# Performance work log

Hardware: AMD Instinct MI355X
Metric: run time of the kernel (lower is better)

Reference implementation:

```python
import jax, jax.numpy as jnp
import numpy as np
from jax import lax

DIM = 256; NH = 8; WS = 4; HD = DIM // NH  # head_dim=32
LH = 4; HH = 4; L_DIM = LH * HD; H_DIM = HH * HD  # 128 each
SCALE = HD ** -0.5


def conv2d(x, w, b, padding=0, groups=1):
    y = lax.conv_general_dilated(x, w, (1, 1), [(padding, padding)] * 2,
                                 feature_group_count=groups,
                                 dimension_numbers=('NCHW', 'OIHW', 'NCHW'))
    return y + b[None, :, None, None]


def dsc(x, dww, dwb, pww, pwb):
    # depthwise 3x3 (pad 1) + pointwise 1x1, both with bias
    y = conv2d(x, dww, dwb, padding=1, groups=x.shape[1])
    return conv2d(y, pww, pwb)


def setup_inputs() -> dict:
    key = jax.random.key(0)
    ks = jax.random.split(key, 16)
    p = lambda k, s: jax.random.normal(k, s, jnp.float32) * 0.02
    B, H, W = 8, 96, 96
    return {
        'x': jax.random.normal(ks[0], (B, DIM, H, W), jnp.float32),
        'restore_w': p(ks[1], (DIM, DIM // (WS * WS), 1, 1)), 'restore_b': jnp.zeros((DIM,), jnp.float32),
        'lq_dw_w': p(ks[2], (DIM, 1, 3, 3)), 'lq_dw_b': jnp.zeros((DIM,), jnp.float32),
        'lq_pw_w': p(ks[3], (L_DIM, DIM, 1, 1)), 'lq_pw_b': jnp.zeros((L_DIM,), jnp.float32),
        'lkv_dw_w': p(ks[4], (DIM, 1, 3, 3)), 'lkv_dw_b': jnp.zeros((DIM,), jnp.float32),
        'lkv_pw_w': p(ks[5], (2 * L_DIM, DIM, 1, 1)), 'lkv_pw_b': jnp.zeros((2 * L_DIM,), jnp.float32),
        'lproj_dw_w': p(ks[6], (L_DIM, 1, 3, 3)), 'lproj_dw_b': jnp.zeros((L_DIM,), jnp.float32),
        'lproj_pw_w': p(ks[7], (L_DIM, L_DIM, 1, 1)), 'lproj_pw_b': jnp.zeros((L_DIM,), jnp.float32),
        'hqkv_dw_w': p(ks[8], (DIM, 1, 3, 3)), 'hqkv_dw_b': jnp.zeros((DIM,), jnp.float32),
        'hqkv_pw_w': p(ks[9], (3 * H_DIM, DIM, 1, 1)), 'hqkv_pw_b': jnp.zeros((3 * H_DIM,), jnp.float32),
        'hproj_dw_w': p(ks[10], (H_DIM, 1, 3, 3)), 'hproj_dw_b': jnp.zeros((H_DIM,), jnp.float32),
        'hproj_pw_w': p(ks[11], (H_DIM, H_DIM, 1, 1)), 'hproj_pw_b': jnp.zeros((H_DIM,), jnp.float32),
    }


def reference(x, restore_w, restore_b,
              lq_dw_w, lq_dw_b, lq_pw_w, lq_pw_b,
              lkv_dw_w, lkv_dw_b, lkv_pw_w, lkv_pw_b,
              lproj_dw_w, lproj_dw_b, lproj_pw_w, lproj_pw_b,
              hqkv_dw_w, hqkv_dw_b, hqkv_pw_w, hqkv_pw_b,
              hproj_dw_w, hproj_dw_b, hproj_pw_w, hproj_pw_b):
    B, C, H, W = x.shape
    hg, wg = H // WS, W // WS
    # ---- low/high feature split (avg-pool + PixelShuffle fallback branch) ----
    low = jnp.mean(x.reshape(B, C, hg, WS, wg, WS), axis=(3, 5))  # [B,C,hg,wg]
    c_out = C // (WS * WS)
    lu = low.reshape(B, c_out, WS, WS, hg, wg)
    lu = lu.transpose(0, 1, 4, 2, 5, 3).reshape(B, c_out, H, W)  # PixelShuffle(WS)
    high = conv2d(lu, restore_w, restore_b) - x
    # ---- low-frequency (global) attention: q at full res, kv at pooled res ----
    lq = dsc(x, lq_dw_w, lq_dw_b, lq_pw_w, lq_pw_b)
    lq = lq.reshape(B, LH, HD, H * W).transpose(0, 1, 3, 2)  # [B,LH,HW,HD]
    lkv = dsc(low, lkv_dw_w, lkv_dw_b, lkv_pw_w, lkv_pw_b)
    lkv = lkv.reshape(B, 2, LH, HD, hg * wg).transpose(1, 0, 2, 4, 3)
    lk, lv = lkv[0], lkv[1]  # [B,LH,hg*wg,HD]
    l_attn = jax.nn.softmax(jnp.einsum('bhqd,bhkd->bhqk', lq, lk) * SCALE, axis=-1)
    lx = jnp.einsum('bhqk,bhkd->bhqd', l_attn, lv)  # [B,LH,HW,HD]
    lx = lx.transpose(0, 1, 3, 2).reshape(B, L_DIM, H, W)
    lx = dsc(lx, lproj_dw_w, lproj_dw_b, lproj_pw_w, lproj_pw_b)
    # ---- high-frequency (windowed local) attention ----
    qkv = dsc(high, hqkv_dw_w, hqkv_dw_b, hqkv_pw_w, hqkv_pw_b)
    qkv = qkv.reshape(B, 3 * HH, HD, hg, WS, wg, WS)
    qkv = qkv.transpose(0, 3, 5, 1, 4, 6, 2).reshape(B, hg * wg, 3, HH, WS * WS, HD)
    qkv = qkv.transpose(2, 0, 1, 3, 4, 5)
    hq, hk, hv = qkv[0], qkv[1], qkv[2]  # [B,G,HH,ws2,HD]
    h_attn = jax.nn.softmax(jnp.einsum('bgnqd,bgnkd->bgnqk', hq, hk) * SCALE, axis=-1)
    ho = jnp.einsum('bgnqk,bgnkd->bgnqd', h_attn, hv)  # [B,G,HH,ws2,HD]
    ho = ho.transpose(0, 1, 3, 2, 4).reshape(B, hg, wg, WS, WS, H_DIM)
    ho = ho.transpose(0, 1, 3, 2, 4, 5).reshape(B, H, W, H_DIM).transpose(0, 3, 1, 2)
    hx = dsc(ho, hproj_dw_w, hproj_dw_b, hproj_pw_w, hproj_pw_b)
    return jnp.concatenate([lx, hx], axis=1)  # [B,DIM,H,W]
```

## Files before the change

### kernel.cpp

```cpp
#include <hip/hip_runtime.h>


#define SCALE_F 0.17677669529663687f

typedef unsigned short u16;
typedef __attribute__((ext_vector_type(8))) short bf16x8;
typedef __attribute__((ext_vector_type(4))) float f32x4;
typedef __attribute__((ext_vector_type(8))) u16 u16x8;
typedef __attribute__((ext_vector_type(4))) u16 u16x4;

static __device__ __forceinline__ u16 f2bf(float f) {
    unsigned u = __float_as_uint(f);
    return (u16)((u + 0x7FFF + ((u >> 16) & 1)) >> 16);
}
static __device__ __forceinline__ float bf2f(u16 v) {
    return __uint_as_float((unsigned)v << 16);
}
static __device__ __forceinline__ float ldf(float v) { return v; }
static __device__ __forceinline__ float ldf(u16 v)   { return bf2f(v); }

__global__ __launch_bounds__(256) void pool_kernel(const float* __restrict__ x,
                                                   float* __restrict__ low) {
    int o = blockIdx.x * 256 + threadIdx.x;
    int wg = o % 24;
    int t  = o / 24;
    int hg = t % 24;
    int bc = t / 24;
    const float* xp = x + (size_t)bc * 9216 + (hg * 4) * 96 + wg * 4;
    float s = 0.f;
#pragma unroll
    for (int r = 0; r < 4; r++) {
        float4 v = *(const float4*)(xp + r * 96);
        s += (v.x + v.y) + (v.z + v.w);
    }
    low[o] = s * (1.f / 16.f);
}

__global__ __launch_bounds__(256) void high_kernel(const float* __restrict__ x,
                                                   const float* __restrict__ low,
                                                   const float* __restrict__ rw,
                                                   const float* __restrict__ rb,
                                                   u16* __restrict__ high) {
    int px = blockIdx.x * 256 + threadIdx.x;
    int cg = blockIdx.y;
    int b  = blockIdx.z;
    int h = px / 96, w = px % 96;
    int sub = (h & 3) * 4 + (w & 3);
    const float* lp = low + ((size_t)b * 256 + sub) * 576 + (h >> 2) * 24 + (w >> 2);
    float lv[16];
#pragma unroll
    for (int co = 0; co < 16; co++) lv[co] = lp[(size_t)co * 16 * 576];
    const float* xp = x    + ((size_t)b * 256 + cg * 64) * 9216 + px;
    u16*         hp = high + ((size_t)b * 256 + cg * 64) * 9216 + px;
#pragma unroll 4
    for (int cl = 0; cl < 64; cl++) {
        int c = cg * 64 + cl;
        float a = rb[c] - xp[(size_t)cl * 9216];
#pragma unroll
        for (int co = 0; co < 16; co++)
            a = fmaf(rw[c * 16 + co], lv[co], a);
        hp[(size_t)cl * 9216] = f2bf(a);
    }
}

__global__ __launch_bounds__(256) void wcvt_kernel(const float* __restrict__ s0,
                                                   const float* __restrict__ s1,
                                                   const float* __restrict__ s2,
                                                   const float* __restrict__ s3,
                                                   const float* __restrict__ s4,
                                                   u16* __restrict__ W) {
    int i = blockIdx.x * 256 + threadIdx.x;
    float v;
    if      (i < 32768)  v = s0[i];
    else if (i < 98304)  v = s1[i - 32768];
    else if (i < 114688) v = s2[i - 98304];
    else if (i < 212992) v = s3[i - 114688];
    else                 v = s4[i - 212992];
    W[i] = f2bf(v);
}

template <int C, int IMH, int IMW, typename TIN>
__global__ __launch_bounds__(256) void dw_kernel(const TIN* __restrict__ in,
                                                 const float* __restrict__ dww,
                                                 const float* __restrict__ dwb,
                                                 u16* __restrict__ Y) {
    constexpr int HW = IMH * IMW;
    constexpr int NSTRIP = HW / 8;
    const int strip = blockIdx.x * 32 + (threadIdx.x >> 3);
    if (strip >= NSTRIP) return;
    const int icq = threadIdx.x & 7;
    const int icg = blockIdx.y, b = blockIdx.z;
    const int ic  = icg * 8 + icq;
    const int px0 = strip * 8;
    const int h   = px0 / IMW, w0 = px0 % IMW;

    const TIN* ip = in + ((size_t)b * C + ic) * HW;
    float r[3][8], lh[3], rh[3];
#pragma unroll
    for (int dr = 0; dr < 3; dr++) {
        int hh = h + dr - 1;
        if (hh < 0 || hh >= IMH) {
#pragma unroll
            for (int j = 0; j < 8; j++) r[dr][j] = 0.f;
            lh[dr] = 0.f; rh[dr] = 0.f;
        } else {
            const TIN* rp = ip + hh * IMW + w0;
            if constexpr (sizeof(TIN) == 4) {
                float4 a = *(const float4*)rp;
                float4 c = *(const float4*)(rp + 4);
                r[dr][0] = a.x; r[dr][1] = a.y; r[dr][2] = a.z; r[dr][3] = a.w;
                r[dr][4] = c.x; r[dr][5] = c.y; r[dr][6] = c.z; r[dr][7] = c.w;
            } else {
                u16x8 a = *(const u16x8*)rp;
#pragma unroll
                for (int j = 0; j < 8; j++) r[dr][j] = bf2f(a[j]);
            }
            lh[dr] = (w0 > 0)           ? ldf(rp[-1]) : 0.f;
            rh[dr] = (w0 + 8 < IMW)     ? ldf(rp[8])  : 0.f;
        }
    }
    const float* wp = dww + ic * 9;
    float wv[9];
#pragma unroll
    for (int t = 0; t < 9; t++) wv[t] = wp[t];
    const float b0 = dwb[ic];

    u16* op = Y + (((size_t)b * (C / 8) + icg) * HW + px0) * 8 + icq;
#pragma unroll
    for (int j = 0; j < 8; j++) {
        float y = b0;
#pragma unroll
        for (int dr = 0; dr < 3; dr++) {
            float l = (j == 0) ? lh[dr] : r[dr][j - 1];
            float m = r[dr][j];
            float rr = (j == 7) ? rh[dr] : r[dr][j + 1];
            y = fmaf(wv[dr * 3 + 0], l, y);
            y = fmaf(wv[dr * 3 + 1], m, y);
            y = fmaf(wv[dr * 3 + 2], rr, y);
        }
        op[j * 8] = f2bf(y);
    }
}

template <int IC, int M, typename TOUT, int MODE>
__global__ __launch_bounds__(256) void pw_gemm(const u16* __restrict__ Y,
                                               const u16* __restrict__ Wmat,
                                               const float* __restrict__ bias,
                                               TOUT* __restrict__ out,
                                               int totc, int ocoff,
                                               u16* __restrict__ qkout,
                                               u16* __restrict__ vout) {
    const int tid  = threadIdx.x;
    const int wave = tid >> 6, lane = tid & 63;
    const int col  = lane & 15, oct = lane >> 4;
    const int mw   = (wave & 1) * 64, nw = (wave >> 1) * 64;
    const int px0    = blockIdx.x * 128;
    const int octile = blockIdx.y;
    const int b      = blockIdx.z;

    __shared__ union {
        struct { u16 W[128 * 72]; u16 Y[8 * 128 * 8]; } g;
        u16 stage[4][64 * 72];
    } lds;
    u16* const Wlds = lds.g.W;
    u16* const Ylds = lds.g.Y;

    f32x4 acc[4][4];
    const f32x4 zero = {0.f, 0.f, 0.f, 0.f};
#pragma unroll
    for (int i = 0; i < 4; i++)
#pragma unroll
        for (int j = 0; j < 4; j++) acc[i][j] = zero;

    const u16* Yb = Y + (size_t)b * (IC / 8) * M * 8;

    for (int kc = 0; kc < IC; kc += 64) {
        __syncthreads();
#pragma unroll
        for (int i = 0; i < 4; i++) {
            int c = tid + i * 256;
            int r = c >> 3, seg = c & 7;
            u16x8 v = *(const u16x8*)(Wmat + (size_t)(octile * 128 + r) * IC + kc + seg * 8);
            *(u16x8*)&Wlds[r * 72 + seg * 8] = v;
        }
#pragma unroll
        for (int i = 0; i < 4; i++) {
            int c = tid + i * 256;
            int ig = c >> 7, pl = c & 127;
            int px = px0 + pl; if (px > M - 1) px = M - 1;
            u16x8 v = *(const u16x8*)(Yb + ((size_t)(kc / 8 + ig) * M + px) * 8);
            *(u16x8*)&Ylds[(ig * 128 + pl) * 8] = v;
        }
        __syncthreads();
#pragma unroll
        for (int kcs = 0; kcs < 2; kcs++) {
            bf16x8 Af[4], Bf[4];
#pragma unroll
            for (int mt = 0; mt < 4; mt++)
                Af[mt] = *(const bf16x8*)&Wlds[(mw + mt * 16 + col) * 72 + kcs * 32 + oct * 8];
#pragma unroll
            for (int nt = 0; nt < 4; nt++)
                Bf[nt] = *(const bf16x8*)&Ylds[((kcs * 4 + oct) * 128 + nw + nt * 16 + col) * 8];
#pragma unroll
            for (int mt = 0; mt < 4; mt++)
#pragma unroll
                for (int nt = 0; nt < 4; nt++)
                    acc[mt][nt] = __builtin_amdgcn_mfma_f32_16x16x32_bf16(
                        Af[mt], Bf[nt], acc[mt][nt], 0, 0, 0);
        }
    }
    if constexpr (MODE == 1) {
        __syncthreads();
        u16* const stg = lds.stage[wave];
#pragma unroll
        for (int mt = 0; mt < 4; mt++)
#pragma unroll
            for (int nt = 0; nt < 4; nt++) {
                u16x4 pk;
#pragma unroll
                for (int i = 0; i < 4; i++) {
                    int oc = octile * 128 + mw + mt * 16 + oct * 4 + i;
                    pk[i] = f2bf(acc[mt][nt][i] + bias[oc]);
                }
                *(u16x4*)&stg[(nt * 16 + col) * 72 + mt * 16 + oct * 4] = pk;
            }
        __syncthreads();
        if (octile < 2) {
            const int p4 = lane >> 2, piece = lane & 3;
#pragma unroll
            for (int pp = 0; pp < 4; pp++) {
                int pl = pp * 16 + p4;
                int px = px0 + nw + pl;
                int h = px / 96, w = px - h * 96;
                int g = (h >> 2) * 24 + (w >> 2);
                int q = (h & 3) * 4 + (w & 3);
                size_t base = (((size_t)b * 576 + g) * 16 + q) * 256
                            + (size_t)(octile * 128 + mw);
#pragma unroll
                for (int half = 0; half < 2; half++) {
                    u16x8 v = *(const u16x8*)&stg[pl * 72 + half * 32 + piece * 8];
                    *(u16x8*)&qkout[base + half * 32 + piece * 8] = v;
                }
            }
        } else {
#pragma unroll
            for (int it = 0; it < 16; it++) {
                int pl0 = it * 4;
                int px = px0 + nw + pl0;
                int h = px / 96, w = px - h * 96;
                int g = (h >> 2) * 24 + (w >> 2);
                int qrow = h & 3;
                int vc = mw + lane;
                u16x4 pk;
#pragma unroll
                for (int j = 0; j < 4; j++) pk[j] = stg[(pl0 + j) * 72 + lane];
                *(u16x4*)&vout[(((size_t)b * 576 + g) * 128 + vc) * 16 + qrow * 4] = pk;
            }
        }
        return;
    }
#pragma unroll
    for (int mt = 0; mt < 4; mt++) {
#pragma unroll
        for (int i = 0; i < 4; i++) {
            int ocl = mw + mt * 16 + oct * 4 + i;
            int oc  = octile * 128 + ocl;
            float bv = bias[oc];
            TOUT* op = out + ((size_t)b * totc + ocoff + oc) * M;
#pragma unroll
            for (int nt = 0; nt < 4; nt++) {
                int px = px0 + nw + nt * 16 + col;
                if (px < M) {
                    float v = acc[mt][nt][i] + bv;
                    if constexpr (sizeof(TOUT) == 2) op[px] = (TOUT)f2bf(v);
                    else                             op[px] = v;
                }
            }
        }
    }
}

__global__ __launch_bounds__(256) void low_attn_mfma(const u16* __restrict__ lq,
                                                     const u16* __restrict__ lkv,
                                                     u16* __restrict__ o) {
    const int qtile = blockIdx.x, head = blockIdx.y, b = blockIdx.z;
    const int tid  = threadIdx.x;
    const int wave = tid >> 6, lane = tid & 63;
    const int col  = lane & 15, oct = lane >> 4;

    __shared__ u16 Klds[96][56];
    __shared__ u16 Vlds[32][104];
    __shared__ u16 Plds[4][16][56];

    const size_t qb  = ((size_t)b * 128 + head * 32) * 9216;
    const size_t kb  = ((size_t)b * 256 + head * 32) * 576;
    const size_t vb  = kb + (size_t)128 * 576;
    const int    q0w = qtile * 256 + wave * 64;

    bf16x8 Qf[4];
#pragma unroll
    for (int qt = 0; qt < 4; qt++)
#pragma unroll
        for (int j = 0; j < 8; j++)
            Qf[qt][j] = (short)lq[qb + (size_t)(oct * 8 + j) * 9216 + q0w + qt * 16 + col];

    bf16x8 ones;
#pragma unroll
    for (int j = 0; j < 8; j++) ones[j] = (short)0x3F80;

    f32x4 Oacc[4][2], Lacc[4];
    const f32x4 zero = {0.f, 0.f, 0.f, 0.f};
#pragma unroll
    for (int qt = 0; qt < 4; qt++) {
        Oacc[qt][0] = zero; Oacc[qt][1] = zero; Lacc[qt] = zero;
    }

    for (int ph = 0; ph < 6; ph++) {
        __syncthreads();
        const int k0 = ph * 96;
#pragma unroll
        for (int i = 0; i < 3; i++) {
            int idx = tid + i * 256;
            int d  = idx / 24;
            int kq = (idx % 24) * 4;
            u16x4 kv = *(const u16x4*)(lkv + kb + (size_t)d * 576 + k0 + kq);
            Klds[kq + 0][d] = kv.x;
            Klds[kq + 1][d] = kv.y;
            Klds[kq + 2][d] = kv.z;
            Klds[kq + 3][d] = kv.w;
            *(u16x4*)&Vlds[d][kq] = *(const u16x4*)(lkv + vb + (size_t)d * 576 + k0 + kq);
        }
        __syncthreads();

        for (int kc = 0; kc < 96; kc += 32) {
            bf16x8 Kf0 = *(const bf16x8*)&Klds[kc + col][oct * 8];
            bf16x8 Kf1 = *(const bf16x8*)&Klds[kc + 16 + col][oct * 8];
            bf16x8 Vf0 = *(const bf16x8*)&Vlds[col][kc + oct * 8];
            bf16x8 Vf1 = *(const bf16x8*)&Vlds[16 + col][kc + oct * 8];
#pragma unroll
            for (int qt = 0; qt < 4; qt++) {
                f32x4 S0 = __builtin_amdgcn_mfma_f32_16x16x32_bf16(Qf[qt], Kf0, zero, 0, 0, 0);
                f32x4 S1 = __builtin_amdgcn_mfma_f32_16x16x32_bf16(Qf[qt], Kf1, zero, 0, 0, 0);
#pragma unroll
                for (int i = 0; i < 4; i++) {
                    Plds[wave][oct * 4 + i][col]      = f2bf(__expf(S0[i] * SCALE_F));
                    Plds[wave][oct * 4 + i][16 + col] = f2bf(__expf(S1[i] * SCALE_F));
                }
                bf16x8 Pf = *(const bf16x8*)&Plds[wave][col][oct * 8];
                Oacc[qt][0] = __builtin_amdgcn_mfma_f32_16x16x32_bf16(Pf, Vf0, Oacc[qt][0], 0, 0, 0);
                Oacc[qt][1] = __builtin_amdgcn_mfma_f32_16x16x32_bf16(Pf, Vf1, Oacc[qt][1], 0, 0, 0);
                Lacc[qt]    = __builtin_amdgcn_mfma_f32_16x16x32_bf16(Pf, ones, Lacc[qt], 0, 0, 0);
            }
        }
    }

#pragma unroll
    for (int qt = 0; qt < 4; qt++) {
        f32x4 rl;
#pragma unroll
        for (int i = 0; i < 4; i++) rl[i] = 1.f / Lacc[qt][i];
#pragma unroll
        for (int dh = 0; dh < 2; dh++)
#pragma unroll
            for (int i = 0; i < 4; i++)
                o[qb + (size_t)(dh * 16 + col) * 9216 + q0w + qt * 16 + oct * 4 + i] =
                    f2bf(Oacc[qt][dh][i] * rl[i]);
    }
}

__global__ __launch_bounds__(256) void high_attn_mfma(const u16* __restrict__ qk,
                                                      const u16* __restrict__ v,
                                                      u16* __restrict__ ho) {
    const int wave = threadIdx.x >> 6, lane = threadIdx.x & 63;
    const int col = lane & 15, oct = lane >> 4;
    const int gidx = blockIdx.x * 4 + wave;
    const int b = gidx / 576, g = gidx % 576;

    __shared__ u16 Plds[4][16][36];
    for (int i = lane; i < 16 * 20; i += 64) {
        Plds[wave][i / 20][16 + i % 20] = 0;
    }
    const u16* qkw = qk + (size_t)gidx * 16 * 256;
    const u16* vw  = v  + (size_t)gidx * 128 * 16;
    const int px0  = ((g / 24) * 4) * 96 + (g % 24) * 4;
    u16* ob = ho + (size_t)b * 128 * 9216 + px0;
    const int qy = col >> 2, qx = col & 3;

    const f32x4 zero = {0.f, 0.f, 0.f, 0.f};
    bf16x8 ones;
#pragma unroll
    for (int j = 0; j < 8; j++) ones[j] = (short)0x3F80;

#pragma unroll
    for (int hd = 0; hd < 4; hd++) {
        bf16x8 Qf = *(const bf16x8*)(qkw + col * 256 + hd * 32 + oct * 8);
        bf16x8 Kf = *(const bf16x8*)(qkw + col * 256 + 128 + hd * 32 + oct * 8);
        f32x4 S = __builtin_amdgcn_mfma_f32_16x16x32_bf16(Qf, Kf, zero, 0, 0, 0);
#pragma unroll
        for (int i = 0; i < 4; i++)
            Plds[wave][oct * 4 + i][col] = f2bf(__expf(S[i] * SCALE_F));
        bf16x8 Pf = *(const bf16x8*)&Plds[wave][col][oct * 8];
        bf16x8 Vf0 = *(const bf16x8*)(vw + (hd * 32 + col) * 16 + oct * 8);
        bf16x8 Vf1 = *(const bf16x8*)(vw + (hd * 32 + 16 + col) * 16 + oct * 8);
        f32x4 O0 = __builtin_amdgcn_mfma_f32_16x16x32_bf16(Vf0, Pf, zero, 0, 0, 0);
        f32x4 O1 = __builtin_amdgcn_mfma_f32_16x16x32_bf16(Vf1, Pf, zero, 0, 0, 0);
        f32x4 Ld = __builtin_amdgcn_mfma_f32_16x16x32_bf16(ones, Pf, zero, 0, 0, 0);
        float rl = 1.f / Ld[0];
#pragma unroll
        for (int i = 0; i < 4; i++) {
            ob[(size_t)(hd * 32 + oct * 4 + i) * 9216 + qy * 96 + qx]      = f2bf(O0[i] * rl);
            ob[(size_t)(hd * 32 + 16 + oct * 4 + i) * 9216 + qy * 96 + qx] = f2bf(O1[i] * rl);
        }
    }
}

extern "C" void kernel_launch(void* const* d_in, const int* in_sizes, int n_in,
                              void* d_out, int out_size, void* d_ws, size_t ws_size,
                              hipStream_t stream) {
    const float* x         = (const float*)d_in[0];
    const float* restore_w = (const float*)d_in[1];
    const float* restore_b = (const float*)d_in[2];
    const float* lq_dw_w   = (const float*)d_in[3];
    const float* lq_dw_b   = (const float*)d_in[4];
    const float* lq_pw_w   = (const float*)d_in[5];
    const float* lq_pw_b   = (const float*)d_in[6];
    const float* lkv_dw_w  = (const float*)d_in[7];
    const float* lkv_dw_b  = (const float*)d_in[8];
    const float* lkv_pw_w  = (const float*)d_in[9];
    const float* lkv_pw_b  = (const float*)d_in[10];
    const float* lpr_dw_w  = (const float*)d_in[11];
    const float* lpr_dw_b  = (const float*)d_in[12];
    const float* lpr_pw_w  = (const float*)d_in[13];
    const float* lpr_pw_b  = (const float*)d_in[14];
    const float* hq_dw_w   = (const float*)d_in[15];
    const float* hq_dw_b   = (const float*)d_in[16];
    const float* hq_pw_w   = (const float*)d_in[17];
    const float* hq_pw_b   = (const float*)d_in[18];
    const float* hp_dw_w   = (const float*)d_in[19];
    const float* hp_dw_b   = (const float*)d_in[20];
    const float* hp_pw_w   = (const float*)d_in[21];
    const float* hp_pw_b   = (const float*)d_in[22];
    float* out = (float*)d_out;
    char*  wsb = (char*)d_ws;

    u16*   Wbf    = (u16*)  (wsb + 0);
    float* low    = (float*)(wsb + 524288);
    u16*   highbf = (u16*)  (wsb + 5242880);
    u16*   ho     = (u16*)  (wsb + 5242880);
    u16*   Yhproj = (u16*)  (wsb + 24117248);
    u16*   Ylq    = (u16*)  (wsb + 80740352);
    u16*   Yhqkv  = (u16*)  (wsb + 80740352);
    u16*   lqbf   = (u16*)  (wsb + 118489088);
    u16*   QKwin  = (u16*)  (wsb + 118489088);
    u16*   Vwin   = (u16*)  (wsb + 156237824);
    u16*   Ylkv   = (u16*)  (wsb + 137363456);
    u16*   lkvbf  = (u16*)  (wsb + 139722752);
    u16*   attnL  = (u16*)  (wsb + 142082048);
    u16*   Ylproj = (u16*)  (wsb + 160956416);

    const u16* wlq    = Wbf;
    const u16* wlkv   = Wbf + 32768;
    const u16* wlproj = Wbf + 98304;
    const u16* whqkv  = Wbf + 114688;
    const u16* whproj = Wbf + 212992;

    wcvt_kernel<<<896, 256, 0, stream>>>(lq_pw_w, lkv_pw_w, lpr_pw_w, hq_pw_w, hp_pw_w, Wbf);
    pool_kernel<<<4608, 256, 0, stream>>>(x, low);
    high_kernel<<<dim3(36, 4, 8), 256, 0, stream>>>(x, low, restore_w, restore_b, highbf);

    dw_kernel<256, 96, 96, float><<<dim3(36, 32, 8), 256, 0, stream>>>(x, lq_dw_w, lq_dw_b, Ylq);
    pw_gemm<256, 9216, u16, 0><<<dim3(72, 1, 8), 256, 0, stream>>>(
        Ylq, wlq, lq_pw_b, lqbf, 128, 0, nullptr, nullptr);

    dw_kernel<256, 24, 24, float><<<dim3(3, 32, 8), 256, 0, stream>>>(low, lkv_dw_w, lkv_dw_b, Ylkv);
    pw_gemm<256, 576, u16, 0><<<dim3(5, 2, 8), 256, 0, stream>>>(
        Ylkv, wlkv, lkv_pw_b, lkvbf, 256, 0, nullptr, nullptr);

    low_attn_mfma<<<dim3(36, 4, 8), 256, 0, stream>>>(lqbf, lkvbf, attnL);

    dw_kernel<128, 96, 96, u16><<<dim3(36, 16, 8), 256, 0, stream>>>(attnL, lpr_dw_w, lpr_dw_b, Ylproj);
    pw_gemm<128, 9216, float, 0><<<dim3(72, 1, 8), 256, 0, stream>>>(
        Ylproj, wlproj, lpr_pw_b, out, 256, 0, nullptr, nullptr);

    dw_kernel<256, 96, 96, u16><<<dim3(36, 32, 8), 256, 0, stream>>>(highbf, hq_dw_w, hq_dw_b, Yhqkv);
    pw_gemm<256, 9216, u16, 1><<<dim3(72, 3, 8), 256, 0, stream>>>(
        Yhqkv, whqkv, hq_pw_b, QKwin, 384, 0, QKwin, Vwin);

    high_attn_mfma<<<1152, 256, 0, stream>>>(QKwin, Vwin, ho);

    dw_kernel<128, 96, 96, u16><<<dim3(36, 16, 8), 256, 0, stream>>>(ho, hp_dw_w, hp_dw_b, Yhproj);
    pw_gemm<128, 9216, float, 0><<<dim3(72, 1, 8), 256, 0, stream>>>(
        Yhproj, whproj, hp_pw_b, out, 256, 128, nullptr, nullptr);
}
```

Before: 543.0 us.

## Prefetch next K/V chunk into registers and pack P stores in low-res attention

The low-frequency attention kernel now loads the next 96-key chunk of K and V from global memory into registers while the current chunk is being computed, so global load latency overlaps the MFMA work. The softmax exponent now uses exp2 with a pre-multiplied log2(e) scale. The two bf16 probabilities are packed with a single v_cvt_pk_bf16_f32 and written as one 32-bit store. The key columns are interleaved (2*col and 2*col+1) both in the P tile and in the V layout, so the PV contraction stays consistent. The cost is extra registers for the prefetch buffers and more complex index math.

```diff
diff --git a/kernel.cpp b/kernel.cpp
--- a/kernel.cpp
+++ b/kernel.cpp
@@ -2,6 +2,7 @@
 
 
 #define SCALE_F 0.17677669529663687f
+#define SCALE_L2E 0.2550349f
 
 typedef unsigned short u16;
 typedef __attribute__((ext_vector_type(8))) short bf16x8;
@@ -290,13 +291,23 @@
 
     __shared__ u16 Klds[96][56];
     __shared__ u16 Vlds[32][104];
-    __shared__ u16 Plds[4][16][56];
+    __shared__ u16 Plds[4][16][40];
 
     const size_t qb  = ((size_t)b * 128 + head * 32) * 9216;
     const size_t kb  = ((size_t)b * 256 + head * 32) * 576;
     const size_t vb  = kb + (size_t)128 * 576;
     const int    q0w = qtile * 256 + wave * 64;
 
+    int sd[3], skq[3], sv0[3];
+#pragma unroll
+    for (int i = 0; i < 3; i++) {
+        int idx = tid + i * 256;
+        sd[i]  = idx / 24;
+        skq[i] = (idx % 24) * 4;
+        int r  = skq[i] & 31;
+        sv0[i] = (skq[i] >> 5) * 32 + ((r & 15) << 1) + (r >> 4);
+    }
+
     bf16x8 Qf[4];
 #pragma unroll
     for (int qt = 0; qt < 4; qt++)
@@ -315,22 +326,36 @@
         Oacc[qt][0] = zero; Oacc[qt][1] = zero; Lacc[qt] = zero;
     }
 
+    u16x4 kr[3], vr[3];
+#pragma unroll
+    for (int i = 0; i < 3; i++) {
+        kr[i] = *(const u16x4*)(lkv + kb + (size_t)sd[i] * 576 + skq[i]);
+        vr[i] = *(const u16x4*)(lkv + vb + (size_t)sd[i] * 576 + skq[i]);
+    }
+
     for (int ph = 0; ph < 6; ph++) {
         __syncthreads();
-        const int k0 = ph * 96;
 #pragma unroll
         for (int i = 0; i < 3; i++) {
-            int idx = tid + i * 256;
-            int d  = idx / 24;
-            int kq = (idx % 24) * 4;
-            u16x4 kv = *(const u16x4*)(lkv + kb + (size_t)d * 576 + k0 + kq);
-            Klds[kq + 0][d] = kv.x;
-            Klds[kq + 1][d] = kv.y;
-            Klds[kq + 2][d] = kv.z;
-            Klds[kq + 3][d] = kv.w;
-            *(u16x4*)&Vlds[d][kq] = *(const u16x4*)(lkv + vb + (size_t)d * 576 + k0 + kq);
+            Klds[skq[i] + 0][sd[i]] = kr[i].x;
+            Klds[skq[i] + 1][sd[i]] = kr[i].y;
+            Klds[skq[i] + 2][sd[i]] = kr[i].z;
+            Klds[skq[i] + 3][sd[i]] = kr[i].w;
+            u16* vp = &Vlds[sd[i]][0];
+            vp[sv0[i] + 0] = vr[i].x;
+            vp[sv0[i] + 2] = vr[i].y;
+            vp[sv0[i] + 4] = vr[i].z;
+            vp[sv0[i] + 6] = vr[i].w;
         }
         __syncthreads();
+        if (ph < 5) {
+            const int k0 = (ph + 1) * 96;
+#pragma unroll
+            for (int i = 0; i < 3; i++) {
+                kr[i] = *(const u16x4*)(lkv + kb + (size_t)sd[i] * 576 + k0 + skq[i]);
+                vr[i] = *(const u16x4*)(lkv + vb + (size_t)sd[i] * 576 + k0 + skq[i]);
+            }
+        }
 
         for (int kc = 0; kc < 96; kc += 32) {
             bf16x8 Kf0 = *(const bf16x8*)&Klds[kc + col][oct * 8];
@@ -343,8 +368,11 @@
                 f32x4 S1 = __builtin_amdgcn_mfma_f32_16x16x32_bf16(Qf[qt], Kf1, zero, 0, 0, 0);
 #pragma unroll
                 for (int i = 0; i < 4; i++) {
-                    Plds[wave][oct * 4 + i][col]      = f2bf(__expf(S0[i] * SCALE_F));
-                    Plds[wave][oct * 4 + i][16 + col] = f2bf(__expf(S1[i] * SCALE_F));
+                    float e0 = exp2f(S0[i] * SCALE_L2E);
+                    float e1 = exp2f(S1[i] * SCALE_L2E);
+                    unsigned pk;
+                    asm("v_cvt_pk_bf16_f32 %0, %1, %2" : "=v"(pk) : "v"(e0), "v"(e1));
+                    ((unsigned*)&Plds[wave][oct * 4 + i][0])[col] = pk;
                 }
                 bf16x8 Pf = *(const bf16x8*)&Plds[wave][col][oct * 8];
                 Oacc[qt][0] = __builtin_amdgcn_mfma_f32_16x16x32_bf16(Pf, Vf0, Oacc[qt][0], 0, 0, 0);
```

Result: no change. 548.5 us (+1.0%).
